# Performance work log

Hardware: AMD Instinct MI355X
Metric: run time of the kernel (lower is better)

## Reference

```python
import jax, jax.numpy as jnp
import numpy as np

NUM_NODES = 16
HSZ = 512
BSZ = 2048


def setup_inputs() -> dict:
    key = jax.random.key(0)
    ks = jax.random.split(key, 5)
    s = 0.02
    return {
        "graphs": jax.random.normal(ks[0], (BSZ, NUM_NODES, HSZ), dtype=jnp.float32),
        "W1": jax.random.normal(ks[1], (NUM_NODES, HSZ, HSZ), dtype=jnp.float32) * s,
        "b1": jnp.zeros((NUM_NODES, HSZ), dtype=jnp.float32),
        "W2": jax.random.normal(ks[2], (NUM_NODES, HSZ, HSZ), dtype=jnp.float32) * s,
        "b2": jnp.zeros((NUM_NODES, HSZ), dtype=jnp.float32),
        "Wg": jax.random.normal(ks[3], (NUM_NODES * HSZ, NUM_NODES), dtype=jnp.float32) * s,
        "bg": jnp.zeros((NUM_NODES,), dtype=jnp.float32),
    }


def reference(graphs, W1, b1, W2, b2, Wg, bg):
    bsz, num_nodes, hsz = graphs.shape
    # Per-node expert MLPs as one batched GEMM over the node axis (fused form
    # of the Python loop over ExpertModel instances).
    h = jax.nn.relu(jnp.einsum('bni,nih->bnh', graphs, W1) + b1)  # (bsz, n, hid)
    outs = jnp.einsum('bnh,nho->bno', h, W2) + b2                 # (bsz, n, out=hsz)
    # torch.cat(outputs, dim=-1).view(bsz, hsz, num_nodes): a raw reshape of the
    # concatenated (bsz, num_nodes*hsz) buffer -- NOT a transpose. Keep it faithful.
    cat = outs.reshape(bsz, num_nodes * hsz).reshape(bsz, hsz, num_nodes)
    # Gating over the flattened graph
    logits = graphs.reshape(bsz, num_nodes * hsz) @ Wg + bg       # (bsz, n)
    expert_probs = jax.nn.softmax(logits, axis=-1)[:, None, :]    # (bsz, 1, n)
    combined = (expert_probs * cat).sum(axis=-1)                  # (bsz, hsz)
    return combined, expert_probs
```

## Files before the change

### kernel.cpp

```cpp
#include <hip/hip_runtime.h>
#include <hip/hip_bf16.h>


typedef __attribute__((ext_vector_type(8))) short bf16x8;
typedef __attribute__((ext_vector_type(4))) float f32x4;

#define OFF_W1T  (0u)
#define OFF_W2T  (8388608u)
#define OFF_H    (16777216u)
#define OFF_PART (50331648u)
#define OFF_PROB (52428800u)

__device__ __forceinline__ void gl2lds16(const void* g, void* l) {
  __builtin_amdgcn_global_load_lds(
      (const __attribute__((address_space(1))) void*)g,
      (__attribute__((address_space(3))) void*)l, 16, 0, 0);
}

__device__ __forceinline__ void cvt16v(const float* __restrict__ src,
                                       bf16x8& lo, bf16x8& hi) {
  float f[16];
  *(float4*)(f + 0)  = *(const float4*)(src + 0);
  *(float4*)(f + 4)  = *(const float4*)(src + 4);
  *(float4*)(f + 8)  = *(const float4*)(src + 8);
  *(float4*)(f + 12) = *(const float4*)(src + 12);
  __hip_bfloat16 t[16];
#pragma unroll
  for (int e = 0; e < 16; e++) t[e] = __float2bfloat16(f[e]);
  lo = *(const bf16x8*)t;
  hi = *(const bf16x8*)(t + 8);
}

__global__ void transpose_kernel(const float* __restrict__ W1,
                                 const float* __restrict__ W2,
                                 __hip_bfloat16* __restrict__ W1t,
                                 __hip_bfloat16* __restrict__ W2t) {
  __shared__ __hip_bfloat16 tile[32][33];
  const int n = blockIdx.z & 15;
  const float* src = (blockIdx.z >> 4) ? W2 : W1;
  __hip_bfloat16* dst = (blockIdx.z >> 4) ? W2t : W1t;
  src += (size_t)n * 262144;
  dst += (size_t)n * 262144;
  const int h0 = blockIdx.x * 32, k0 = blockIdx.y * 32;
  const int tx = threadIdx.x, ty = threadIdx.y;
#pragma unroll
  for (int i = 0; i < 32; i += 8)
    tile[ty + i][tx] = __float2bfloat16(src[(size_t)(k0 + ty + i) * 512 + h0 + tx]);
  __syncthreads();
#pragma unroll
  for (int i = 0; i < 32; i += 8)
    dst[(size_t)(h0 + ty + i) * 512 + k0 + tx] = tile[tx][ty + i];
}

__global__ __launch_bounds__(256) void gating_kernel(
    const float* __restrict__ graphs,
    const float* __restrict__ Wg,
    float* __restrict__ partial) {
  __shared__ char smem[24832];
  const int tid = threadIdx.x, lane = tid & 63, wave = tid >> 6;
  const int bid = blockIdx.x;
  const int n = bid & 15, rb = bid >> 4;
  const int q = lane >> 4, l15 = lane & 15;

  char* Bt = smem + 8192;
#pragma unroll
  for (int i = 0; i < 2; i++) {
    int k = i * 256 + tid;
    const float* wr_ = Wg + (size_t)(n * 512 + k) * 16;
    float f[16];
    *(float4*)(f + 0)  = *(const float4*)(wr_ + 0);
    *(float4*)(f + 4)  = *(const float4*)(wr_ + 4);
    *(float4*)(f + 8)  = *(const float4*)(wr_ + 8);
    *(float4*)(f + 12) = *(const float4*)(wr_ + 12);
#pragma unroll
    for (int j = 0; j < 16; j++)
      *(__hip_bfloat16*)(Bt + j * 1040 + k * 2) = __float2bfloat16(f[j]);
  }
  __syncthreads();

  const int arow = lane >> 1, ahalf = (lane & 1) * 16;
  const float* Ag = graphs + (size_t)(rb * 32) * 8192 + n * 512 + wave * 128;
  char* Aw = smem + wave * 2048;

  f32x4 acc[2] = {};
  for (int ks = 0; ks < 4; ks++) {
    bf16x8 lo, hi;
    cvt16v(Ag + (size_t)arow * 8192 + ks * 32 + ahalf, lo, hi);
    char* d = Aw + arow * 64 + ahalf * 2;
    *(bf16x8*)d = lo;
    *(bf16x8*)(d + 16) = hi;
    bf16x8 bv = *(const bf16x8*)(Bt + l15 * 1040 + (wave * 128 + ks * 32 + q * 8) * 2);
#pragma unroll
    for (int im = 0; im < 2; im++) {
      bf16x8 av = *(const bf16x8*)(Aw + (im * 16 + l15) * 64 + q * 16);
      acc[im] = __builtin_amdgcn_mfma_f32_16x16x32_bf16(av, bv, acc[im], 0, 0, 0);
    }
  }
#pragma unroll
  for (int im = 0; im < 2; im++)
#pragma unroll
    for (int r = 0; r < 4; r++)
      *(float*)(smem + wave * 2048 + (im * 16 + q * 4 + r) * 64 + l15 * 4) = acc[im][r];
  __syncthreads();
#pragma unroll
  for (int i = 0; i < 2; i++) {
    int c = i * 256 + tid;
    int rrow = c >> 4, j = c & 15;
    float s = 0.f;
#pragma unroll
    for (int w = 0; w < 4; w++) s += *(const float*)(smem + w * 2048 + rrow * 64 + j * 4);
    partial[((size_t)n * 2048 + rb * 32 + rrow) * 16 + j] = s;
  }
}

__global__ void softmax_kernel(const float* __restrict__ partial,
                               const float* __restrict__ bg,
                               float* __restrict__ probs,
                               float* __restrict__ probs_out) {
  const int r = blockIdx.x * 256 + threadIdx.x;
  float s[16];
#pragma unroll
  for (int j = 0; j < 16; j++) s[j] = 0.f;
  for (int nn = 0; nn < 16; nn++) {
    const float4* p = (const float4*)(partial + ((size_t)nn * 2048 + r) * 16);
#pragma unroll
    for (int c = 0; c < 4; c++) {
      float4 v = p[c];
      s[c * 4 + 0] += v.x; s[c * 4 + 1] += v.y;
      s[c * 4 + 2] += v.z; s[c * 4 + 3] += v.w;
    }
  }
  float mx = -1e30f;
#pragma unroll
  for (int j = 0; j < 16; j++) { s[j] += bg[j]; mx = fmaxf(mx, s[j]); }
  float sum = 0.f;
#pragma unroll
  for (int j = 0; j < 16; j++) { s[j] = __expf(s[j] - mx); sum += s[j]; }
  float inv = 1.f / sum;
#pragma unroll
  for (int j = 0; j < 16; j++) s[j] *= inv;
  float4* pw = (float4*)(probs + (size_t)r * 16);
  float4* ow = (float4*)(probs_out + (size_t)r * 16);
#pragma unroll
  for (int c = 0; c < 4; c++) {
    float4 v = make_float4(s[c*4], s[c*4+1], s[c*4+2], s[c*4+3]);
    pw[c] = v; ow[c] = v;
  }
}

__device__ __forceinline__ void decode_bid(int bid, int& nblk, int& mblk, int& n) {
  int x8 = bid & 7;
  nblk = (bid >> 3) & 3;
  int pair = (bid >> 5) * 8 + x8;
  mblk = pair >> 4;
  n = pair & 15;
}

__global__ __launch_bounds__(256, 4) void gemm1_kernel(
    const float* __restrict__ graphs,
    const __hip_bfloat16* __restrict__ W1t,
    const float* __restrict__ b1,
    __hip_bfloat16* __restrict__ h) {
  __shared__ char smem[36864];
  const int tid = threadIdx.x, lane = tid & 63, wave = tid >> 6;
  int nblk, mblk, n;
  decode_bid(blockIdx.x, nblk, mblk, n);
  const int wm = (wave >> 1) * 64, wn = (wave & 1) * 64;
  const int q = lane >> 4, l15 = lane & 15;
  const int lrow = lane >> 3, lcol = lane & 7;
  const int swz = (lcol ^ lrow) * 8;
  const int xr = l15 & 7;
  const int arow = tid >> 1, ahalf = (tid & 1) * 32;
  const int arx = arow & 7;

  const float* Ag = graphs + (size_t)(mblk * 128) * 8192 + n * 512;
  const __hip_bfloat16* Bg = W1t + (size_t)n * 262144 + (size_t)(nblk * 128) * 512;

  f32x4 acc[4][4] = {};
  for (int ks = 0; ks < 8; ks++) {
    const int k0 = ks * 64;
    const float* asrc = Ag + (size_t)arow * 8192 + k0 + ahalf;
    float f[32];
#pragma unroll
    for (int j = 0; j < 8; j++) *(float4*)(f + j * 4) = *(const float4*)(asrc + j * 4);
    __hip_bfloat16 t[32];
#pragma unroll
    for (int e = 0; e < 32; e++) t[e] = __float2bfloat16(f[e]);
    char* abase = smem + arow * 128;
#pragma unroll
    for (int j = 0; j < 4; j++) {
      int c = (ahalf >> 3) + j;
      *(bf16x8*)(abase + ((c ^ arx) * 16)) = *(const bf16x8*)(t + j * 8);
    }
#pragma unroll
    for (int i = 0; i < 4; i++) {
      const int r = i * 32 + wave * 8 + lrow;
      gl2lds16(Bg + (size_t)r * 512 + k0 + swz,
               smem + 16384 + i * 4096 + wave * 1024 + lane * 16);
    }
    __syncthreads();
#pragma unroll
    for (int hh = 0; hh < 2; hh++) {
      const int co = ((q + hh * 4) ^ xr) * 16;
      bf16x8 av[4], bv[4];
#pragma unroll
      for (int im = 0; im < 4; im++)
        av[im] = *(const bf16x8*)(smem + (wm + im * 16 + l15) * 128 + co);
#pragma unroll
      for (int in = 0; in < 4; in++)
        bv[in] = *(const bf16x8*)(smem + 16384 + (wn + in * 16 + l15) * 128 + co);
#pragma unroll
      for (int im = 0; im < 4; im++)
#pragma unroll
        for (int in = 0; in < 4; in++)
          acc[im][in] = __builtin_amdgcn_mfma_f32_16x16x32_bf16(av[im], bv[in], acc[im][in], 0, 0, 0);
    }
    __syncthreads();
  }

  float bias[4];
#pragma unroll
  for (int in = 0; in < 4; in++)
    bias[in] = b1[n * 512 + nblk * 128 + wn + in * 16 + l15];
  char* epi = smem + wave * 9216;
#pragma unroll
  for (int im = 0; im < 4; im++)
#pragma unroll
    for (int in = 0; in < 4; in++)
#pragma unroll
      for (int r = 0; r < 4; r++) {
        float v = acc[im][in][r] + bias[in];
        v = fmaxf(v, 0.f);
        int rl = im * 16 + q * 4 + r;
        int cl = in * 16 + l15;
        *(__hip_bfloat16*)(epi + rl * 144 + cl * 2) = __float2bfloat16(v);
      }
  __syncthreads();
  __hip_bfloat16* Hg = h + (size_t)(mblk * 128 + wm) * 8192 + n * 512 + nblk * 128 + wn;
#pragma unroll
  for (int it = 0; it < 8; it++) {
    int rl = it * 8 + (lane >> 3);
    int cl = (lane & 7) * 8;
    bf16x8 v = *(const bf16x8*)(epi + rl * 144 + cl * 2);
    *(bf16x8*)(Hg + (size_t)rl * 8192 + cl) = v;
  }
}

__global__ __launch_bounds__(256, 4) void gemm2_kernel(
    const __hip_bfloat16* __restrict__ hbuf,
    const __hip_bfloat16* __restrict__ W2t,
    const float* __restrict__ b2,
    const float* __restrict__ probs,
    float* __restrict__ out) {
  __shared__ char smem[32768];
  const int tid = threadIdx.x, lane = tid & 63, wave = tid >> 6;
  int nblk, mblk, n;
  decode_bid(blockIdx.x, nblk, mblk, n);
  const int wm = (wave >> 1) * 64, wn = (wave & 1) * 64;
  const int q = lane >> 4, l15 = lane & 15;
  const int lrow = lane >> 3, lcol = lane & 7;
  const int swz = (lcol ^ lrow) * 8;
  const int xr = l15 & 7;

  const __hip_bfloat16* Ag = hbuf + (size_t)(mblk * 128) * 8192 + n * 512;
  const __hip_bfloat16* Bg = W2t + (size_t)n * 262144 + (size_t)(nblk * 128) * 512;

  f32x4 acc[4][4] = {};
  for (int ks = 0; ks < 8; ks++) {
    const int k0 = ks * 64;
#pragma unroll
    for (int i = 0; i < 4; i++) {
      const int r = i * 32 + wave * 8 + lrow;
      gl2lds16(Ag + (size_t)r * 8192 + k0 + swz, smem + i * 4096 + wave * 1024 + lane * 16);
      gl2lds16(Bg + (size_t)r * 512 + k0 + swz,
               smem + 16384 + i * 4096 + wave * 1024 + lane * 16);
    }
    __syncthreads();
#pragma unroll
    for (int hh = 0; hh < 2; hh++) {
      const int co = ((q + hh * 4) ^ xr) * 16;
      bf16x8 av[4], bv[4];
#pragma unroll
      for (int im = 0; im < 4; im++)
        av[im] = *(const bf16x8*)(smem + (wm + im * 16 + l15) * 128 + co);
#pragma unroll
      for (int in = 0; in < 4; in++)
        bv[in] = *(const bf16x8*)(smem + 16384 + (wn + in * 16 + l15) * 128 + co);
#pragma unroll
      for (int im = 0; im < 4; im++)
#pragma unroll
        for (int in = 0; in < 4; in++)
          acc[im][in] = __builtin_amdgcn_mfma_f32_16x16x32_bf16(av[im], bv[in], acc[im][in], 0, 0, 0);
    }
    __syncthreads();
  }

  float bias[4];
#pragma unroll
  for (int in = 0; in < 4; in++)
    bias[in] = b2[n * 512 + nblk * 128 + wn + in * 16 + l15];
  float* comb = (float*)smem;
#pragma unroll
  for (int im = 0; im < 4; im++)
#pragma unroll
    for (int r = 0; r < 4; r++) {
      int rl = wm + im * 16 + q * 4 + r;
      float pv = probs[(size_t)(mblk * 128 + rl) * 16 + l15];
#pragma unroll
      for (int in = 0; in < 4; in++) {
        float v = (acc[im][in][r] + bias[in]) * pv;
        v += __shfl_xor(v, 1);
        v += __shfl_xor(v, 2);
        v += __shfl_xor(v, 4);
        v += __shfl_xor(v, 8);
        if (l15 == 0) comb[rl * 8 + (wn >> 4) + in] = v;
      }
    }
  __syncthreads();
  if (tid < 128) {
    float4 v0 = *(const float4*)(comb + tid * 8);
    float4 v1 = *(const float4*)(comb + tid * 8 + 4);
    float* orow = out + (size_t)(mblk * 128 + tid) * 512 + n * 32 + nblk * 8;
    *(float4*)orow = v0;
    *(float4*)(orow + 4) = v1;
  }
}

extern "C" void kernel_launch(void* const* d_in, const int* in_sizes, int n_in,
                              void* d_out, int out_size, void* d_ws, size_t ws_size,
                              hipStream_t stream) {
  const float* graphs = (const float*)d_in[0];
  const float* W1 = (const float*)d_in[1];
  const float* b1 = (const float*)d_in[2];
  const float* W2 = (const float*)d_in[3];
  const float* b2 = (const float*)d_in[4];
  const float* Wg = (const float*)d_in[5];
  const float* bg = (const float*)d_in[6];
  float* out = (float*)d_out;

  char* ws = (char*)d_ws;
  __hip_bfloat16* W1t = (__hip_bfloat16*)(ws + OFF_W1T);
  __hip_bfloat16* W2t = (__hip_bfloat16*)(ws + OFF_W2T);
  __hip_bfloat16* hb  = (__hip_bfloat16*)(ws + OFF_H);
  float* partial = (float*)(ws + OFF_PART);
  float* probs   = (float*)(ws + OFF_PROB);

  transpose_kernel<<<dim3(16, 16, 32), dim3(32, 8), 0, stream>>>(W1, W2, W1t, W2t);
  gating_kernel<<<1024, 256, 0, stream>>>(graphs, Wg, partial);
  softmax_kernel<<<8, 256, 0, stream>>>(partial, bg, probs, out + 2048 * 512);
  gemm1_kernel<<<1024, 256, 0, stream>>>(graphs, W1t, b1, hb);
  gemm2_kernel<<<1024, 256, 0, stream>>>(hb, W2t, b2, probs, out);
}
```

Measured before the change: 220.1 us.

## Fuse gating GEMM into gemm1 and register-prefetch tiles in both GEMMs

Drops the separate gating kernel. The gating logits are now computed inside gemm1 by the nblk==0 blocks, which reuse the bf16 graph tiles already staged in LDS together with a small Wg tile, so the second full fp32 read of graphs goes away. Both GEMMs also replace direct global-to-LDS loads with register prefetch of the next K-slice, stored into LDS through a swizzle, to overlap loads with MFMA. Launch bounds drop from 4 to 3 blocks per CU to make room for the extra registers. The risks are imbalance, since only a quarter of gemm1 blocks do the gating work, and lower occupancy.

```diff
diff --git a/kernel.cpp b/kernel.cpp
--- a/kernel.cpp
+++ b/kernel.cpp
@@ -10,26 +10,6 @@
 #define OFF_H    (16777216u)
 #define OFF_PART (50331648u)
 #define OFF_PROB (52428800u)
-
-__device__ __forceinline__ void gl2lds16(const void* g, void* l) {
-  __builtin_amdgcn_global_load_lds(
-      (const __attribute__((address_space(1))) void*)g,
-      (__attribute__((address_space(3))) void*)l, 16, 0, 0);
-}
-
-__device__ __forceinline__ void cvt16v(const float* __restrict__ src,
-                                       bf16x8& lo, bf16x8& hi) {
-  float f[16];
-  *(float4*)(f + 0)  = *(const float4*)(src + 0);
-  *(float4*)(f + 4)  = *(const float4*)(src + 4);
-  *(float4*)(f + 8)  = *(const float4*)(src + 8);
-  *(float4*)(f + 12) = *(const float4*)(src + 12);
-  __hip_bfloat16 t[16];
-#pragma unroll
-  for (int e = 0; e < 16; e++) t[e] = __float2bfloat16(f[e]);
-  lo = *(const bf16x8*)t;
-  hi = *(const bf16x8*)(t + 8);
-}
 
 __global__ void transpose_kernel(const float* __restrict__ W1,
                                  const float* __restrict__ W2,
@@ -52,67 +32,6 @@
     dst[(size_t)(h0 + ty + i) * 512 + k0 + tx] = tile[tx][ty + i];
 }
 
-__global__ __launch_bounds__(256) void gating_kernel(
-    const float* __restrict__ graphs,
-    const float* __restrict__ Wg,
-    float* __restrict__ partial) {
-  __shared__ char smem[24832];
-  const int tid = threadIdx.x, lane = tid & 63, wave = tid >> 6;
-  const int bid = blockIdx.x;
-  const int n = bid & 15, rb = bid >> 4;
-  const int q = lane >> 4, l15 = lane & 15;
-
-  char* Bt = smem + 8192;
-#pragma unroll
-  for (int i = 0; i < 2; i++) {
-    int k = i * 256 + tid;
-    const float* wr_ = Wg + (size_t)(n * 512 + k) * 16;
-    float f[16];
-    *(float4*)(f + 0)  = *(const float4*)(wr_ + 0);
-    *(float4*)(f + 4)  = *(const float4*)(wr_ + 4);
-    *(float4*)(f + 8)  = *(const float4*)(wr_ + 8);
-    *(float4*)(f + 12) = *(const float4*)(wr_ + 12);
-#pragma unroll
-    for (int j = 0; j < 16; j++)
-      *(__hip_bfloat16*)(Bt + j * 1040 + k * 2) = __float2bfloat16(f[j]);
-  }
-  __syncthreads();
-
-  const int arow = lane >> 1, ahalf = (lane & 1) * 16;
-  const float* Ag = graphs + (size_t)(rb * 32) * 8192 + n * 512 + wave * 128;
-  char* Aw = smem + wave * 2048;
-
-  f32x4 acc[2] = {};
-  for (int ks = 0; ks < 4; ks++) {
-    bf16x8 lo, hi;
-    cvt16v(Ag + (size_t)arow * 8192 + ks * 32 + ahalf, lo, hi);
-    char* d = Aw + arow * 64 + ahalf * 2;
-    *(bf16x8*)d = lo;
-    *(bf16x8*)(d + 16) = hi;
-    bf16x8 bv = *(const bf16x8*)(Bt + l15 * 1040 + (wave * 128 + ks * 32 + q * 8) * 2);
-#pragma unroll
-    for (int im = 0; im < 2; im++) {
-      bf16x8 av = *(const bf16x8*)(Aw + (im * 16 + l15) * 64 + q * 16);
-      acc[im] = __builtin_amdgcn_mfma_f32_16x16x32_bf16(av, bv, acc[im], 0, 0, 0);
-    }
-  }
-#pragma unroll
-  for (int im = 0; im < 2; im++)
-#pragma unroll
-    for (int r = 0; r < 4; r++)
-      *(float*)(smem + wave * 2048 + (im * 16 + q * 4 + r) * 64 + l15 * 4) = acc[im][r];
-  __syncthreads();
-#pragma unroll
-  for (int i = 0; i < 2; i++) {
-    int c = i * 256 + tid;
-    int rrow = c >> 4, j = c & 15;
-    float s = 0.f;
-#pragma unroll
-    for (int w = 0; w < 4; w++) s += *(const float*)(smem + w * 2048 + rrow * 64 + j * 4);
-    partial[((size_t)n * 2048 + rb * 32 + rrow) * 16 + j] = s;
-  }
-}
-
 __global__ void softmax_kernel(const float* __restrict__ partial,
                                const float* __restrict__ bg,
                                float* __restrict__ probs,
@@ -156,49 +75,73 @@
   n = pair & 15;
 }
 
-__global__ __launch_bounds__(256, 4) void gemm1_kernel(
+__global__ __launch_bounds__(256, 3) void gemm1_kernel(
     const float* __restrict__ graphs,
     const __hip_bfloat16* __restrict__ W1t,
+    const float* __restrict__ Wg,
     const float* __restrict__ b1,
-    __hip_bfloat16* __restrict__ h) {
+    __hip_bfloat16* __restrict__ h,
+    float* __restrict__ partial) {
   __shared__ char smem[36864];
   const int tid = threadIdx.x, lane = tid & 63, wave = tid >> 6;
   int nblk, mblk, n;
   decode_bid(blockIdx.x, nblk, mblk, n);
   const int wm = (wave >> 1) * 64, wn = (wave & 1) * 64;
   const int q = lane >> 4, l15 = lane & 15;
-  const int lrow = lane >> 3, lcol = lane & 7;
-  const int swz = (lcol ^ lrow) * 8;
   const int xr = l15 & 7;
-  const int arow = tid >> 1, ahalf = (tid & 1) * 32;
-  const int arx = arow & 7;
+  const int row2 = tid >> 1, half = tid & 1;
+  const int rx = row2 & 7;
+  const int wk = tid >> 2, wj = (tid & 3) * 4;
+  const bool do_gate = (nblk == 0);
+  const int gt0 = (wave & 1) * 2;
 
   const float* Ag = graphs + (size_t)(mblk * 128) * 8192 + n * 512;
   const __hip_bfloat16* Bg = W1t + (size_t)n * 262144 + (size_t)(nblk * 128) * 512;
+  const float* Wgg = Wg + (size_t)(n * 512) * 16;
+
+  const float* asrc = Ag + (size_t)row2 * 8192 + half * 32;
+  const __hip_bfloat16* bsrc = Bg + (size_t)row2 * 512 + half * 32;
+
+  float af[32];
+  uint4 bq[4];
+  float4 wgq = make_float4(0.f, 0.f, 0.f, 0.f);
+#pragma unroll
+  for (int j = 0; j < 8; j++) *(float4*)(af + j * 4) = *(const float4*)(asrc + j * 4);
+#pragma unroll
+  for (int j = 0; j < 4; j++) bq[j] = ((const uint4*)bsrc)[j];
+  if (do_gate) wgq = *(const float4*)(Wgg + (size_t)wk * 16 + wj);
 
   f32x4 acc[4][4] = {};
+  f32x4 accg[2] = {};
   for (int ks = 0; ks < 8; ks++) {
-    const int k0 = ks * 64;
-    const float* asrc = Ag + (size_t)arow * 8192 + k0 + ahalf;
-    float f[32];
-#pragma unroll
-    for (int j = 0; j < 8; j++) *(float4*)(f + j * 4) = *(const float4*)(asrc + j * 4);
     __hip_bfloat16 t[32];
 #pragma unroll
-    for (int e = 0; e < 32; e++) t[e] = __float2bfloat16(f[e]);
-    char* abase = smem + arow * 128;
+    for (int e = 0; e < 32; e++) t[e] = __float2bfloat16(af[e]);
+    char* abase = smem + row2 * 128;
+    char* bbase = smem + 16384 + row2 * 128;
 #pragma unroll
     for (int j = 0; j < 4; j++) {
-      int c = (ahalf >> 3) + j;
-      *(bf16x8*)(abase + ((c ^ arx) * 16)) = *(const bf16x8*)(t + j * 8);
-    }
-#pragma unroll
-    for (int i = 0; i < 4; i++) {
-      const int r = i * 32 + wave * 8 + lrow;
-      gl2lds16(Bg + (size_t)r * 512 + k0 + swz,
-               smem + 16384 + i * 4096 + wave * 1024 + lane * 16);
+      int c = half * 4 + j;
+      *(bf16x8*)(abase + ((c ^ rx) * 16)) = *(const bf16x8*)(t + j * 8);
+      *(uint4*)(bbase + ((c ^ rx) * 16)) = bq[j];
+    }
+    if (do_gate) {
+      __hip_bfloat16 wt[4] = {__float2bfloat16(wgq.x), __float2bfloat16(wgq.y),
+                              __float2bfloat16(wgq.z), __float2bfloat16(wgq.w)};
+#pragma unroll
+      for (int i = 0; i < 4; i++)
+        *(__hip_bfloat16*)(smem + 32768 + (wj + i) * 144 + wk * 2) = wt[i];
     }
     __syncthreads();
+    if (ks < 7) {
+      const int kp = (ks + 1) * 64;
+#pragma unroll
+      for (int j = 0; j < 8; j++)
+        *(float4*)(af + j * 4) = *(const float4*)(asrc + kp + j * 4);
+#pragma unroll
+      for (int j = 0; j < 4; j++) bq[j] = ((const uint4*)(bsrc + kp))[j];
+      if (do_gate) wgq = *(const float4*)(Wgg + (size_t)(kp + wk) * 16 + wj);
+    }
 #pragma unroll
     for (int hh = 0; hh < 2; hh++) {
       const int co = ((q + hh * 4) ^ xr) * 16;
@@ -214,8 +157,23 @@
 #pragma unroll
         for (int in = 0; in < 4; in++)
           acc[im][in] = __builtin_amdgcn_mfma_f32_16x16x32_bf16(av[im], bv[in], acc[im][in], 0, 0, 0);
+      if (do_gate) {
+        bf16x8 wv = *(const bf16x8*)(smem + 32768 + l15 * 144 + (q + hh * 4) * 16);
+        accg[0] = __builtin_amdgcn_mfma_f32_16x16x32_bf16(av[gt0], wv, accg[0], 0, 0, 0);
+        accg[1] = __builtin_amdgcn_mfma_f32_16x16x32_bf16(av[gt0 + 1], wv, accg[1], 0, 0, 0);
+      }
     }
     __syncthreads();
+  }
+
+  if (do_gate) {
+#pragma unroll
+    for (int t2 = 0; t2 < 2; t2++)
+#pragma unroll
+      for (int r = 0; r < 4; r++) {
+        int row = mblk * 128 + wave * 32 + t2 * 16 + q * 4 + r;
+        partial[((size_t)n * 2048 + row) * 16 + l15] = accg[t2][r];
+      }
   }
 
   float bias[4];
@@ -246,7 +204,7 @@
   }
 }
 
-__global__ __launch_bounds__(256, 4) void gemm2_kernel(
+__global__ __launch_bounds__(256, 3) void gemm2_kernel(
     const __hip_bfloat16* __restrict__ hbuf,
     const __hip_bfloat16* __restrict__ W2t,
     const float* __restrict__ b2,
@@ -258,24 +216,41 @@
   decode_bid(blockIdx.x, nblk, mblk, n);
   const int wm = (wave >> 1) * 64, wn = (wave & 1) * 64;
   const int q = lane >> 4, l15 = lane & 15;
-  const int lrow = lane >> 3, lcol = lane & 7;
-  const int swz = (lcol ^ lrow) * 8;
   const int xr = l15 & 7;
+  const int row2 = tid >> 1, half = tid & 1;
+  const int rx = row2 & 7;
 
   const __hip_bfloat16* Ag = hbuf + (size_t)(mblk * 128) * 8192 + n * 512;
   const __hip_bfloat16* Bg = W2t + (size_t)n * 262144 + (size_t)(nblk * 128) * 512;
+  const __hip_bfloat16* asrc = Ag + (size_t)row2 * 8192 + half * 32;
+  const __hip_bfloat16* bsrc = Bg + (size_t)row2 * 512 + half * 32;
+
+  uint4 aq[4], bq[4];
+#pragma unroll
+  for (int j = 0; j < 4; j++) {
+    aq[j] = ((const uint4*)asrc)[j];
+    bq[j] = ((const uint4*)bsrc)[j];
+  }
 
   f32x4 acc[4][4] = {};
   for (int ks = 0; ks < 8; ks++) {
-    const int k0 = ks * 64;
-#pragma unroll
-    for (int i = 0; i < 4; i++) {
-      const int r = i * 32 + wave * 8 + lrow;
-      gl2lds16(Ag + (size_t)r * 8192 + k0 + swz, smem + i * 4096 + wave * 1024 + lane * 16);
-      gl2lds16(Bg + (size_t)r * 512 + k0 + swz,
-               smem + 16384 + i * 4096 + wave * 1024 + lane * 16);
+    char* abase = smem + row2 * 128;
+    char* bbase = smem + 16384 + row2 * 128;
+#pragma unroll
+    for (int j = 0; j < 4; j++) {
+      int c = half * 4 + j;
+      *(uint4*)(abase + ((c ^ rx) * 16)) = aq[j];
+      *(uint4*)(bbase + ((c ^ rx) * 16)) = bq[j];
     }
     __syncthreads();
+    if (ks < 7) {
+      const int kp = (ks + 1) * 64;
+#pragma unroll
+      for (int j = 0; j < 4; j++) {
+        aq[j] = ((const uint4*)(asrc + kp))[j];
+        bq[j] = ((const uint4*)(bsrc + kp))[j];
+      }
+    }
 #pragma unroll
     for (int hh = 0; hh < 2; hh++) {
       const int co = ((q + hh * 4) ^ xr) * 16;
@@ -346,8 +321,7 @@
   float* probs   = (float*)(ws + OFF_PROB);
 
   transpose_kernel<<<dim3(16, 16, 32), dim3(32, 8), 0, stream>>>(W1, W2, W1t, W2t);
-  gating_kernel<<<1024, 256, 0, stream>>>(graphs, Wg, partial);
+  gemm1_kernel<<<1024, 256, 0, stream>>>(graphs, W1t, Wg, b1, hb, partial);
   softmax_kernel<<<8, 256, 0, stream>>>(partial, bg, probs, out + 2048 * 512);
-  gemm1_kernel<<<1024, 256, 0, stream>>>(graphs, W1t, b1, hb);
   gemm2_kernel<<<1024, 256, 0, stream>>>(hb, W2t, b2, probs, out);
 }
```

Measured after the change: 435.5 us. 97.9% more time.

## Fuse gating into gemm1 launch and vectorize weight transpose with 64x64 tiles

Applied to the files above, without the earlier changes.

The gating GEMM blocks are merged into the gemm1 launch as extra blocks (block index >= 1024), so one launch replaces two and the gating work can overlap with gemm1. The softmax launch now comes after this combined kernel, which is fine since gemm1 does not depend on the probabilities. The weight transpose is rewritten to use 64x64 tiles, float4 reads and 16-byte bf16 writes in place of scalar 32x32 tiles, cutting per-element global traffic. The fused kernel keeps gemm1's launch bounds and shared-memory size, so the gating branch may limit occupancy or raise register pressure.

```diff
diff --git a/kernel.cpp b/kernel.cpp
--- a/kernel.cpp
+++ b/kernel.cpp
@@ -31,85 +31,36 @@
   hi = *(const bf16x8*)(t + 8);
 }
 
-__global__ void transpose_kernel(const float* __restrict__ W1,
-                                 const float* __restrict__ W2,
-                                 __hip_bfloat16* __restrict__ W1t,
-                                 __hip_bfloat16* __restrict__ W2t) {
-  __shared__ __hip_bfloat16 tile[32][33];
-  const int n = blockIdx.z & 15;
-  const float* src = (blockIdx.z >> 4) ? W2 : W1;
-  __hip_bfloat16* dst = (blockIdx.z >> 4) ? W2t : W1t;
+__global__ __launch_bounds__(256) void transpose_kernel(
+    const float* __restrict__ W1, const float* __restrict__ W2,
+    __hip_bfloat16* __restrict__ W1t, __hip_bfloat16* __restrict__ W2t) {
+  __shared__ char smem[9216];
+  const int bx = blockIdx.x;
+  const int ht = bx & 7, kt = bx >> 3;
+  const int n = blockIdx.y & 15;
+  const float* src = (blockIdx.y >> 4) ? W2 : W1;
+  __hip_bfloat16* dst = (blockIdx.y >> 4) ? W2t : W1t;
   src += (size_t)n * 262144;
   dst += (size_t)n * 262144;
-  const int h0 = blockIdx.x * 32, k0 = blockIdx.y * 32;
-  const int tx = threadIdx.x, ty = threadIdx.y;
-#pragma unroll
-  for (int i = 0; i < 32; i += 8)
-    tile[ty + i][tx] = __float2bfloat16(src[(size_t)(k0 + ty + i) * 512 + h0 + tx]);
+  const int tid = threadIdx.x;
+  const int hq4 = (tid & 15) * 4, kr = tid >> 4;
+#pragma unroll
+  for (int rr = 0; rr < 4; rr++) {
+    const int kl = rr * 16 + kr;
+    float4 v = *(const float4*)(src + (size_t)(kt * 64 + kl) * 512 + ht * 64 + hq4);
+    __hip_bfloat16 t4[4] = {__float2bfloat16(v.x), __float2bfloat16(v.y),
+                            __float2bfloat16(v.z), __float2bfloat16(v.w)};
+#pragma unroll
+    for (int i = 0; i < 4; i++)
+      *(__hip_bfloat16*)(smem + (hq4 + i) * 144 + kl * 2) = t4[i];
+  }
   __syncthreads();
-#pragma unroll
-  for (int i = 0; i < 32; i += 8)
-    dst[(size_t)(h0 + ty + i) * 512 + k0 + tx] = tile[tx][ty + i];
-}
-
-__global__ __launch_bounds__(256) void gating_kernel(
-    const float* __restrict__ graphs,
-    const float* __restrict__ Wg,
-    float* __restrict__ partial) {
-  __shared__ char smem[24832];
-  const int tid = threadIdx.x, lane = tid & 63, wave = tid >> 6;
-  const int bid = blockIdx.x;
-  const int n = bid & 15, rb = bid >> 4;
-  const int q = lane >> 4, l15 = lane & 15;
-
-  char* Bt = smem + 8192;
-#pragma unroll
-  for (int i = 0; i < 2; i++) {
-    int k = i * 256 + tid;
-    const float* wr_ = Wg + (size_t)(n * 512 + k) * 16;
-    float f[16];
-    *(float4*)(f + 0)  = *(const float4*)(wr_ + 0);
-    *(float4*)(f + 4)  = *(const float4*)(wr_ + 4);
-    *(float4*)(f + 8)  = *(const float4*)(wr_ + 8);
-    *(float4*)(f + 12) = *(const float4*)(wr_ + 12);
-#pragma unroll
-    for (int j = 0; j < 16; j++)
-      *(__hip_bfloat16*)(Bt + j * 1040 + k * 2) = __float2bfloat16(f[j]);
-  }
-  __syncthreads();
-
-  const int arow = lane >> 1, ahalf = (lane & 1) * 16;
-  const float* Ag = graphs + (size_t)(rb * 32) * 8192 + n * 512 + wave * 128;
-  char* Aw = smem + wave * 2048;
-
-  f32x4 acc[2] = {};
-  for (int ks = 0; ks < 4; ks++) {
-    bf16x8 lo, hi;
-    cvt16v(Ag + (size_t)arow * 8192 + ks * 32 + ahalf, lo, hi);
-    char* d = Aw + arow * 64 + ahalf * 2;
-    *(bf16x8*)d = lo;
-    *(bf16x8*)(d + 16) = hi;
-    bf16x8 bv = *(const bf16x8*)(Bt + l15 * 1040 + (wave * 128 + ks * 32 + q * 8) * 2);
-#pragma unroll
-    for (int im = 0; im < 2; im++) {
-      bf16x8 av = *(const bf16x8*)(Aw + (im * 16 + l15) * 64 + q * 16);
-      acc[im] = __builtin_amdgcn_mfma_f32_16x16x32_bf16(av, bv, acc[im], 0, 0, 0);
-    }
-  }
-#pragma unroll
-  for (int im = 0; im < 2; im++)
-#pragma unroll
-    for (int r = 0; r < 4; r++)
-      *(float*)(smem + wave * 2048 + (im * 16 + q * 4 + r) * 64 + l15 * 4) = acc[im][r];
-  __syncthreads();
-#pragma unroll
-  for (int i = 0; i < 2; i++) {
-    int c = i * 256 + tid;
-    int rrow = c >> 4, j = c & 15;
-    float s = 0.f;
-#pragma unroll
-    for (int w = 0; w < 4; w++) s += *(const float*)(smem + w * 2048 + rrow * 64 + j * 4);
-    partial[((size_t)n * 2048 + rb * 32 + rrow) * 16 + j] = s;
+  const int c8 = tid & 7, hr = tid >> 3;
+#pragma unroll
+  for (int rr = 0; rr < 2; rr++) {
+    const int hl = rr * 32 + hr;
+    bf16x8 v = *(const bf16x8*)(smem + hl * 144 + c8 * 16);
+    *(bf16x8*)(dst + (size_t)(ht * 64 + hl) * 512 + kt * 64 + c8 * 8) = v;
   }
 }
 
@@ -156,17 +107,75 @@
   n = pair & 15;
 }
 
-__global__ __launch_bounds__(256, 4) void gemm1_kernel(
+__global__ __launch_bounds__(256, 4) void gemm1_gate_kernel(
     const float* __restrict__ graphs,
     const __hip_bfloat16* __restrict__ W1t,
+    const float* __restrict__ Wg,
     const float* __restrict__ b1,
-    __hip_bfloat16* __restrict__ h) {
+    __hip_bfloat16* __restrict__ h,
+    float* __restrict__ partial) {
   __shared__ char smem[36864];
   const int tid = threadIdx.x, lane = tid & 63, wave = tid >> 6;
+  const int q = lane >> 4, l15 = lane & 15;
+
+  if (blockIdx.x >= 1024) {
+    const int gbid = blockIdx.x - 1024;
+    const int n = gbid & 15, rb = gbid >> 4;
+    char* Bt = smem + 8192;
+#pragma unroll
+    for (int i = 0; i < 2; i++) {
+      int k = i * 256 + tid;
+      const float* wr_ = Wg + (size_t)(n * 512 + k) * 16;
+      float f[16];
+      *(float4*)(f + 0)  = *(const float4*)(wr_ + 0);
+      *(float4*)(f + 4)  = *(const float4*)(wr_ + 4);
+      *(float4*)(f + 8)  = *(const float4*)(wr_ + 8);
+      *(float4*)(f + 12) = *(const float4*)(wr_ + 12);
+#pragma unroll
+      for (int j = 0; j < 16; j++)
+        *(__hip_bfloat16*)(Bt + j * 1040 + k * 2) = __float2bfloat16(f[j]);
+    }
+    __syncthreads();
+
+    const int arow = lane >> 1, ahalf = (lane & 1) * 16;
+    const float* Ag = graphs + (size_t)(rb * 32) * 8192 + n * 512 + wave * 128;
+    char* Aw = smem + wave * 2048;
+
+    f32x4 acc[2] = {};
+    for (int ks = 0; ks < 4; ks++) {
+      bf16x8 lo, hi;
+      cvt16v(Ag + (size_t)arow * 8192 + ks * 32 + ahalf, lo, hi);
+      char* d = Aw + arow * 64 + ahalf * 2;
+      *(bf16x8*)d = lo;
+      *(bf16x8*)(d + 16) = hi;
+      bf16x8 bv = *(const bf16x8*)(Bt + l15 * 1040 + (wave * 128 + ks * 32 + q * 8) * 2);
+#pragma unroll
+      for (int im = 0; im < 2; im++) {
+        bf16x8 av = *(const bf16x8*)(Aw + (im * 16 + l15) * 64 + q * 16);
+        acc[im] = __builtin_amdgcn_mfma_f32_16x16x32_bf16(av, bv, acc[im], 0, 0, 0);
+      }
+    }
+#pragma unroll
+    for (int im = 0; im < 2; im++)
+#pragma unroll
+      for (int r = 0; r < 4; r++)
+        *(float*)(smem + wave * 2048 + (im * 16 + q * 4 + r) * 64 + l15 * 4) = acc[im][r];
+    __syncthreads();
+#pragma unroll
+    for (int i = 0; i < 2; i++) {
+      int c = i * 256 + tid;
+      int rrow = c >> 4, j = c & 15;
+      float s = 0.f;
+#pragma unroll
+      for (int w = 0; w < 4; w++) s += *(const float*)(smem + w * 2048 + rrow * 64 + j * 4);
+      partial[((size_t)n * 2048 + rb * 32 + rrow) * 16 + j] = s;
+    }
+    return;
+  }
+
   int nblk, mblk, n;
   decode_bid(blockIdx.x, nblk, mblk, n);
   const int wm = (wave >> 1) * 64, wn = (wave & 1) * 64;
-  const int q = lane >> 4, l15 = lane & 15;
   const int lrow = lane >> 3, lcol = lane & 7;
   const int swz = (lcol ^ lrow) * 8;
   const int xr = l15 & 7;
@@ -345,9 +354,8 @@
   float* partial = (float*)(ws + OFF_PART);
   float* probs   = (float*)(ws + OFF_PROB);
 
-  transpose_kernel<<<dim3(16, 16, 32), dim3(32, 8), 0, stream>>>(W1, W2, W1t, W2t);
-  gating_kernel<<<1024, 256, 0, stream>>>(graphs, Wg, partial);
+  transpose_kernel<<<dim3(64, 32), 256, 0, stream>>>(W1, W2, W1t, W2t);
+  gemm1_gate_kernel<<<2048, 256, 0, stream>>>(graphs, W1t, Wg, b1, hb, partial);
   softmax_kernel<<<8, 256, 0, stream>>>(partial, bg, probs, out + 2048 * 512);
-  gemm1_kernel<<<1024, 256, 0, stream>>>(graphs, W1t, b1, hb);
   gemm2_kernel<<<1024, 256, 0, stream>>>(hb, W2t, b2, probs, out);
 }
```

Result: faster. 212.7 us (-3.3%).
